# Optimization experiments

Measured on AMD Instinct MI355X. Metric: run time of the kernel, lower is better.

## Reference

```python
import jax, jax.numpy as jnp
import numpy as np

# static config (matches init_kwargs)
C = 64            # dim_split = dim // 4
DIM = 256
HID = 128         # int(dim//4 * mlp_ratio), mlp_ratio=2
S = 64            # state_dim
NH, HD = 16, 4    # GA: num_heads = C // head_dim, head_dim = 4
AK, AP = 11, 5    # att_kernel, att_padding
B, H, W = 8, 28, 28


def conv2d(x, w, pad, stride=1, groups=1, bias=None):
    out = jax.lax.conv_general_dilated(
        x, w, (stride, stride), pad, feature_group_count=groups,
        dimension_numbers=('NCHW', 'OIHW', 'NCHW'))
    if bias is not None:
        out = out + bias[None, :, None, None]
    return out


def pw(x, w, b=None):  # 1x1 conv, w: (O, Cin)
    y = jnp.einsum('oc,bchw->bohw', w, x)
    return y if b is None else y + b[None, :, None, None]


def bn(x, p, eps=1e-5):  # eval-mode BatchNorm2d; p: (4, C) = gamma, beta, mean, var
    g, b, m, v = p
    s = g / jnp.sqrt(v + eps)
    return (x - m[None, :, None, None]) * s[None, :, None, None] + b[None, :, None, None]


def relu6(x):
    return jnp.minimum(jax.nn.relu(x), 6.0)


def maxpool3(x):  # 3x3, stride 1, pad 1
    return jax.lax.reduce_window(x, -jnp.inf, jax.lax.max, (1, 1, 3, 3), (1, 1, 1, 1),
                                 [(0, 0), (0, 0), (1, 1), (1, 1)])


def blurpool(x):  # antialiased_cnns.BlurPool(channels, stride=3), filt_size=4
    a = np.array([1.0, 3.0, 3.0, 1.0])
    filt = np.outer(a, a)
    filt = filt / filt.sum()
    c = x.shape[1]
    w = jnp.asarray(np.tile(filt[None, None], (c, 1, 1, 1)), x.dtype)
    xp = jnp.pad(x, ((0, 0), (0, 0), (1, 2), (1, 2)), mode='reflect')
    return conv2d(xp, w, [(0, 0), (0, 0)], stride=3, groups=c)


def h_transform(x):
    b, c, hs, ws = x.shape
    x = jnp.pad(x, ((0, 0), (0, 0), (0, 0), (0, ws))).reshape(b, c, -1)[..., :-ws]
    return x.reshape(b, c, hs, 2 * ws - 1)


def inv_h_transform(x):
    b, c, hs, _ = x.shape
    x = jnp.pad(x.reshape(b, c, -1), ((0, 0), (0, 0), (0, hs)))
    return x.reshape(b, c, hs, 2 * hs)[..., :hs]


def v_transform(x):
    return h_transform(x.transpose(0, 1, 3, 2)).transpose(0, 1, 3, 2)


def inv_v_transform(x):
    return inv_h_transform(x.transpose(0, 1, 3, 2)).transpose(0, 1, 3, 2)


def _forward(x, dw1_w, dw1_b, bn_dw1, f1_w, f1_b, f2_w, f2_b, g_w, g_b, bn_g,
             dw2_w, dw2_b, hatt1_w, vatt1_w, hatt2_w, vatt2_w, bn_mra,
             bcdt_w, ssd_dw_w, hz_w, out_w, A_param, D_param,
             qkv_w, proj_w, bn_norm4, mlp1_w, bn_mlp, mlp2_w, bn_norm1):
    shortcut = x
    x1, x2, x3, x4 = jnp.split(x, 4, axis=1)

    # --- branch 1: dwconv + star-gated MLP ---
    x1o = bn(conv2d(x1, dw1_w, [(3, 3), (3, 3)], groups=C, bias=dw1_b), bn_dw1)
    x1 = relu6(pw(x1o, f1_w, f1_b)) * pw(x1o, f2_w, f2_b)
    x1 = conv2d(bn(pw(x1, g_w, g_b), bn_g), dw2_w, [(3, 3), (3, 3)], groups=C, bias=dw2_b)

    # --- branch 2: MRA ---
    xt = blurpool(maxpool3(x2))  # (B, C, 10, 10)
    xh1 = conv2d(xt, hatt1_w, [(AP, AP), (1, 1)], groups=C)
    xw1 = conv2d(xt, vatt1_w, [(1, 1), (AP, AP)], groups=C)
    xh2 = inv_h_transform(conv2d(h_transform(xt), hatt2_w, [(AP, AP), (1, 1)], groups=C))
    xw2 = inv_v_transform(conv2d(v_transform(xt), vatt2_w, [(1, 1), (AP, AP)], groups=C))
    att = jax.nn.sigmoid(bn(xh1 + xw1 + xh2 + xw2, bn_mra))
    hs, ws = att.shape[-2], att.shape[-1]
    ri = (jnp.arange(H) * hs) // H  # nearest-neighbor upsampling indices
    ci = (jnp.arange(W) * ws) // W
    x2 = x2 * att[:, :, ri][:, :, :, ci]

    # --- branch 3: HSMSSD (hidden-state-mixer SSD) ---
    L = H * W
    xs = x3.reshape(B, C, L)
    bcdt = conv2d(jnp.einsum('oc,bcl->bol', bcdt_w, xs).reshape(B, 3 * S, H, W),
                  ssd_dw_w, [(1, 1), (1, 1)], groups=3 * S).reshape(B, 3 * S, L)
    Bm, Cm, dt = jnp.split(bcdt, 3, axis=1)              # each (B, S, L)
    A = jax.nn.softmax(dt + A_param[None, :, None], axis=-1)
    h = jnp.einsum('bcl,bsl->bcs', xs, A * Bm)           # (B, C, S)
    h_, z = jnp.split(jnp.einsum('oc,bcs->bos', hz_w, h), 2, axis=1)
    h_ = jnp.einsum('oc,bcs->bos', out_w, h_ * jax.nn.silu(z) + h_ * D_param)
    x3 = jnp.einsum('bcs,bsl->bcl', h_, Cm).reshape(B, C, H, W)

    # --- branch 4: GA full attention + BN residual (stage == 3) ---
    t = x4.reshape(B, C, L).transpose(0, 2, 1)           # (B, N, C)
    qkv = (t @ qkv_w.T).reshape(B, L, 3, NH, HD).transpose(2, 0, 3, 1, 4)
    q, k, v = qkv[0], qkv[1], qkv[2]
    attn = jax.nn.softmax(jnp.einsum('bhnd,bhmd->bhnm', q, k) * HD ** -0.5, axis=-1)
    o = jnp.einsum('bhnm,bhmd->bhnd', attn, v).transpose(0, 2, 1, 3).reshape(B, L, NH * HD)
    x4 = bn(x4 + (o @ proj_w.T).transpose(0, 2, 1).reshape(B, C, H, W), bn_norm4)

    # --- merge + MLP ---
    xa = jnp.concatenate([x1, x2, x3, x4], axis=1)
    m = pw(jax.nn.relu(bn(pw(xa, mlp1_w), bn_mlp)), mlp2_w)
    return shortcut + bn(m, bn_norm1)


def setup_inputs() -> dict:
    key = jax.random.key(0)
    ks = iter(jax.random.split(key, 64))

    def w(shape, s=0.05):
        return jax.random.normal(next(ks), shape, dtype=jnp.float32) * s

    def bnp(c):
        g = 1.0 + 0.1 * jax.random.normal(next(ks), (c,), dtype=jnp.float32)
        b = 0.1 * jax.random.normal(next(ks), (c,), dtype=jnp.float32)
        m = 0.1 * jax.random.normal(next(ks), (c,), dtype=jnp.float32)
        v = 0.5 + jax.random.uniform(next(ks), (c,), dtype=jnp.float32)
        return jnp.stack([g, b, m, v])

    return dict(
        x=jax.random.normal(next(ks), (B, DIM, H, W), dtype=jnp.float32),
        dw1_w=w((C, 1, 7, 7), 0.1), dw1_b=w((C,), 0.02), bn_dw1=bnp(C),
        f1_w=w((HID, C)), f1_b=w((HID,), 0.02),
        f2_w=w((HID, C)), f2_b=w((HID,), 0.02),
        g_w=w((C, HID)), g_b=w((C,), 0.02), bn_g=bnp(C),
        dw2_w=w((C, 1, 7, 7), 0.1), dw2_b=w((C,), 0.02),
        hatt1_w=w((C, 1, AK, 3), 0.1), vatt1_w=w((C, 1, 3, AK), 0.1),
        hatt2_w=w((C, 1, AK, 3), 0.1), vatt2_w=w((C, 1, 3, AK), 0.1),
        bn_mra=bnp(C),
        bcdt_w=w((3 * S, C)), ssd_dw_w=w((3 * S, 1, 3, 3), 0.1),
        hz_w=w((2 * C, C)), out_w=w((C, C)),
        A_param=jax.random.uniform(next(ks), (S,), dtype=jnp.float32, minval=1.0, maxval=16.0),
        D_param=jnp.ones((1,), dtype=jnp.float32),
        qkv_w=w((3 * NH * HD, C)), proj_w=w((C, NH * HD)),
        bn_norm4=bnp(C),
        mlp1_w=w((HID, DIM)), bn_mlp=bnp(HID), mlp2_w=w((DIM, HID)),
        bn_norm1=bnp(DIM),
    )


def reference(x, dw1_w, dw1_b, bn_dw1, f1_w, f1_b, f2_w, f2_b, g_w, g_b, bn_g,
              dw2_w, dw2_b, hatt1_w, vatt1_w, hatt2_w, vatt2_w, bn_mra,
              bcdt_w, ssd_dw_w, hz_w, out_w, A_param, D_param,
              qkv_w, proj_w, bn_norm4, mlp1_w, bn_mlp, mlp2_w, bn_norm1):
    return _forward(x, dw1_w, dw1_b, bn_dw1, f1_w, f1_b, f2_w, f2_b, g_w, g_b, bn_g,
                    dw2_w, dw2_b, hatt1_w, vatt1_w, hatt2_w, vatt2_w, bn_mra,
                    bcdt_w, ssd_dw_w, hz_w, out_w, A_param, D_param,
                    qkv_w, proj_w, bn_norm4, mlp1_w, bn_mlp, mlp2_w, bn_norm1)
```

## Files before the change

kernel.cpp:

```cpp
#include <hip/hip_runtime.h>
#include <hip/hip_bf16.h>
#include <math.h>

#define DEV __device__ __forceinline__

constexpr int B=8, C=64, DIM=256, HID=128, S=64, NH=16, HD=4, LPIX=784;
constexpr int NPIX = B*LPIX;
constexpr int CH   = (NPIX+255)/256;
constexpr int QB   = 12*((NPIX+511)/512);

constexpr size_t OFF_X1O = 0;
constexpr size_t OFF_T1  = OFF_X1O + (size_t)B*C*LPIX;
constexpr size_t OFF_T2  = OFF_T1  + (size_t)B*HID*LPIX;
constexpr size_t OFF_XA  = OFF_T2  + (size_t)B*C*LPIX;
constexpr size_t OFF_BC2 = OFF_XA  + (size_t)B*DIM*LPIX;
constexpr size_t OFF_WGT = OFF_BC2 + (size_t)B*192*LPIX;
constexpr size_t OFF_H   = OFF_WGT + (size_t)B*S*LPIX;
constexpr size_t OFF_HO  = OFF_H   + (size_t)4*B*C*S;
constexpr size_t OFF_QKV = OFF_HO  + (size_t)B*C*S;
constexpr size_t OFF_O   = OFF_QKV + (size_t)3*B*NH*LPIX*HD;
constexpr size_t OFF_LS  = OFF_O   + (size_t)4*B*LPIX*C;
constexpr size_t OFF_MID = OFF_LS  + (size_t)4*B*NH*LPIX;

DEV float bnorm(float x, const float* p, int c, int nc){
  float g=p[c], bb=p[nc+c], m=p[2*nc+c], v=p[3*nc+c];
  return (x-m)*(g*rsqrtf(v+1e-5f))+bb;
}
DEV int refl(int p){ int k=p-1; if(k<0)k=-k; if(k>27)k=54-k; return k; }

DEV bool upix(int blk, int tid, int ngroups, int& grp, int& b, int& l){
  grp = blk % ngroups;
  int gidx = (blk/ngroups)*256 + tid;
  if(gidx >= NPIX) return false;
  b = gidx / LPIX; l = gidx % LPIX;
  return true;
}

DEV void body_dw1t(int bc, int tid, float* xs, const float* X, const float* w, const float* bias, const float* bnp, float* out){
  int c = bc & 63, b = bc >> 6;
  const float* xp = X + ((size_t)(b*DIM+c))*LPIX;
  for(int i=tid;i<34*34;i+=256) xs[i]=0.f;
  __syncthreads();
  for(int i=tid;i<LPIX;i+=256){ int y=i/28, x=i%28; xs[(y+3)*34+(x+3)]=xp[i]; }
  __syncthreads();
  const float* wc = w + (size_t)c*49;
  float bs = bias[c];
  for(int i=tid;i<LPIX;i+=256){
    int y=i/28, x=i%28;
    float s = bs;
    #pragma unroll
    for(int ky=0;ky<7;ky++){
      #pragma unroll
      for(int kx=0;kx<7;kx++)
        s += xs[(y+ky)*34 + x+kx]*wc[ky*7+kx];
    }
    out[((size_t)(b*C+c))*LPIX + i] = bnorm(s,bnp,c,C);
  }
}

DEV void body_branch2(int bc, int tid, float* smem, const float* X,
                      const float* h1w,const float* v1w,const float* h2w,const float* v2w,
                      const float* bnp, float* xa){
  int c = bc & 63, b = bc >> 6;
  float* xs  = smem;
  float* mp  = smem+LPIX;
  float* xt  = smem+2*LPIX;
  float* attv= smem+2*LPIX+100;
  const float* xp = X + ((size_t)(b*DIM+64+c))*LPIX;
  for(int i=tid;i<LPIX;i+=256) xs[i]=xp[i];
  __syncthreads();
  for(int i=tid;i<LPIX;i+=256){
    int y=i/28, x=i%28;
    float m=-1e30f;
    for(int dy=-1;dy<=1;dy++){ int iy=y+dy; if(iy<0||iy>=28) continue;
      for(int dx=-1;dx<=1;dx++){ int ix=x+dx; if(ix<0||ix>=28) continue;
        m=fmaxf(m,xs[iy*28+ix]); } }
    mp[i]=m;
  }
  __syncthreads();
  if(tid<100){
    int ii=tid/10, j=tid%10;
    const float fw[4]={0.125f,0.375f,0.375f,0.125f};
    float s=0;
    for(int ky=0;ky<4;ky++){ int rr=refl(3*ii+ky);
      for(int kx=0;kx<4;kx++){ int cc=refl(3*j+kx);
        s += fw[ky]*fw[kx]*mp[rr*28+cc]; } }
    xt[tid]=s;
  }
  __syncthreads();
  if(tid<100){
    int r=tid/10, j=tid%10;
    float s=0;
    for(int kh=0;kh<11;kh++){ int a=r+kh-5; if(a<0||a>=10) continue;
      for(int kw=0;kw<3;kw++){ int b2=j+kw-1; if(b2<0||b2>=10) continue;
        s+=xt[a*10+b2]*h1w[(size_t)c*33+kh*3+kw]; } }
    for(int kh=0;kh<3;kh++){ int a=r+kh-1; if(a<0||a>=10) continue;
      for(int kw=0;kw<11;kw++){ int b2=j+kw-5; if(b2<0||b2>=10) continue;
        s+=xt[a*10+b2]*v1w[(size_t)c*33+kh*11+kw]; } }
    { int t=20*r+j; int r2=t/19, j2=t%19;
      for(int kh=0;kh<11;kh++){ int a=r2+kh-5; if(a<0||a>=10) continue;
        for(int kw=0;kw<3;kw++){ int b2=j2+kw-1; if(b2<0||b2>=19) continue;
          int i2=19*a+b2; int row=i2/20, col=i2%20;
          if(col<10) s+=xt[row*10+col]*h2w[(size_t)c*33+kh*3+kw]; } } }
    { int t=20*j+r; int p=t%19, q=t/19;
      for(int kh=0;kh<3;kh++){ int a=p+kh-1; if(a<0||a>=19) continue;
        for(int kw=0;kw<11;kw++){ int b2=q+kw-5; if(b2<0||b2>=10) continue;
          int i2=19*b2+a; int row=i2/20, col=i2%20;
          if(col<10) s+=xt[col*10+row]*v2w[(size_t)c*33+kh*11+kw]; } } }
    s = bnorm(s,bnp,c,C);
    attv[tid] = 1.f/(1.f+__expf(-s));
  }
  __syncthreads();
  float* dst = xa + ((size_t)(b*DIM+64+c))*LPIX;
  for(int i=tid;i<LPIX;i+=256){
    int y=i/28, x=i%28;
    float a = attv[((y*10)/28)*10 + (x*10)/28];
    dst[i] = xs[i]*a;
  }
}

DEV void body_qkv(int blk, int tid, const float* X, const float* w, float* qkvb){
  int og = blk % 12;
  int p0 = (blk/12)*512 + tid;
  if(p0 >= NPIX) return;
  int o0 = og*16;
  int b0 = p0/LPIX, l0 = p0%LPIX;
  int p1 = p0 + 256;
  bool has1 = p1 < NPIX;
  int b1 = has1 ? p1/LPIX : b0, l1 = has1 ? p1%LPIX : l0;
  const float* xp0 = X + ((size_t)(b0*DIM+192))*LPIX + l0;
  const float* xp1 = X + ((size_t)(b1*DIM+192))*LPIX + l1;
  float s0[16], s1[16];
  #pragma unroll
  for(int t=0;t<16;t++){ s0[t]=0.f; s1[t]=0.f; }
  for(int c=0;c<C;c+=4){
    float a0=xp0[(size_t)c*LPIX],     a1=xp0[(size_t)(c+1)*LPIX],
          a2=xp0[(size_t)(c+2)*LPIX], a3=xp0[(size_t)(c+3)*LPIX];
    float e0=xp1[(size_t)c*LPIX],     e1=xp1[(size_t)(c+1)*LPIX],
          e2=xp1[(size_t)(c+2)*LPIX], e3=xp1[(size_t)(c+3)*LPIX];
    #pragma unroll
    for(int t=0;t<16;t++){
      const float* wr = w + (size_t)(o0+t)*C + c;
      float w0=wr[0], w1=wr[1], w2=wr[2], w3=wr[3];
      s0[t] += w0*a0 + w1*a1 + w2*a2 + w3*a3;
      s1[t] += w0*e0 + w1*e1 + w2*e2 + w3*e3;
    }
  }
  int which=o0>>6, head0=(o0&63)>>2;
  #pragma unroll
  for(int t4=0;t4<4;t4++){
    float4* dst = (float4*)(qkvb + (size_t)which*B*NH*LPIX*HD + ((size_t)((b0*NH+head0+t4)*LPIX+l0))*HD);
    *dst = make_float4(s0[4*t4],s0[4*t4+1],s0[4*t4+2],s0[4*t4+3]);
  }
  if(has1){
    #pragma unroll
    for(int t4=0;t4<4;t4++){
      float4* dst = (float4*)(qkvb + (size_t)which*B*NH*LPIX*HD + ((size_t)((b1*NH+head0+t4)*LPIX+l1))*HD);
      *dst = make_float4(s1[4*t4],s1[4*t4+1],s1[4*t4+2],s1[4*t4+3]);
    }
  }
}

DEV void body_bcdtssd(int blk, int tid, float* smem, const float* X, const float* w, const float* dww,
                      float* bc2, float* wgt){
  int b = blk/48, og = blk%48; int o0=og*4;
  float* bc1s = smem;
  float* dts1 = smem + 4*LPIX;
  float* red  = smem + 5*LPIX;
  const float* xp = X + ((size_t)(b*DIM+128))*LPIX;
  {
    int l0=tid, l1=tid+256, l2=tid+512;
    float acc0[4]={0,0,0,0}, acc1[4]={0,0,0,0}, acc2[4]={0,0,0,0};
    for(int c=0;c<C;c+=4){
      float x00=xp[(size_t)c*LPIX+l0],     x01=xp[(size_t)(c+1)*LPIX+l0],
            x02=xp[(size_t)(c+2)*LPIX+l0], x03=xp[(size_t)(c+3)*LPIX+l0];
      float x10=xp[(size_t)c*LPIX+l1],     x11=xp[(size_t)(c+1)*LPIX+l1],
            x12=xp[(size_t)(c+2)*LPIX+l1], x13=xp[(size_t)(c+3)*LPIX+l1];
      float x20=xp[(size_t)c*LPIX+l2],     x21=xp[(size_t)(c+1)*LPIX+l2],
            x22=xp[(size_t)(c+2)*LPIX+l2], x23=xp[(size_t)(c+3)*LPIX+l2];
      #pragma unroll
      for(int t=0;t<4;t++){
        const float* wr = w + (size_t)(o0+t)*C + c;
        float w0=wr[0], w1=wr[1], w2=wr[2], w3=wr[3];
        acc0[t] += w0*x00 + w1*x01 + w2*x02 + w3*x03;
        acc1[t] += w0*x10 + w1*x11 + w2*x12 + w3*x13;
        acc2[t] += w0*x20 + w1*x21 + w2*x22 + w3*x23;
      }
    }
    #pragma unroll
    for(int t=0;t<4;t++){
      bc1s[t*LPIX+l0]=acc0[t];
      bc1s[t*LPIX+l1]=acc1[t];
      bc1s[t*LPIX+l2]=acc2[t];
    }
    if(tid<16){
      int l=768+tid;
      float a0=0,a1=0,a2=0,a3=0;
      for(int c=0;c<C;c+=4){
        float x0=xp[(size_t)c*LPIX+l],     x1=xp[(size_t)(c+1)*LPIX+l],
              x2=xp[(size_t)(c+2)*LPIX+l], x3=xp[(size_t)(c+3)*LPIX+l];
        const float* w0p = w + (size_t)(o0+0)*C + c;
        const float* w1p = w + (size_t)(o0+1)*C + c;
        const float* w2p = w + (size_t)(o0+2)*C + c;
        const float* w3p = w + (size_t)(o0+3)*C + c;
        a0 += w0p[0]*x0 + w0p[1]*x1 + w0p[2]*x2 + w0p[3]*x3;
        a1 += w1p[0]*x0 + w1p[1]*x1 + w1p[2]*x2 + w1p[3]*x3;
        a2 += w2p[0]*x0 + w2p[1]*x1 + w2p[2]*x2 + w2p[3]*x3;
        a3 += w3p[0]*x0 + w3p[1]*x1 + w3p[2]*x2 + w3p[3]*x3;
      }
      bc1s[0*LPIX+l]=a0; bc1s[1*LPIX+l]=a1; bc1s[2*LPIX+l]=a2; bc1s[3*LPIX+l]=a3;
    }
  }
  __syncthreads();
  if(og < 32){
    for(int i=tid;i<4*LPIX;i+=256){
      int oo=i/LPIX, l=i%LPIX; int y=l/28, x=l%28;
      const float* p = bc1s + oo*LPIX;
      const float* wk = dww + (size_t)(o0+oo)*9;
      float s=0;
      for(int ky=0;ky<3;ky++){ int iy=y+ky-1; if(iy<0||iy>=28) continue;
        for(int kx=0;kx<3;kx++){ int ix=x+kx-1; if(ix<0||ix>=28) continue;
          s += p[iy*28+ix]*wk[ky*3+kx]; } }
      bc2[((size_t)(b*192+o0+oo))*LPIX + l] = s;
    }
  } else {
    int wv = tid>>6, lane = tid&63;
    for(int oo=0;oo<4;oo++){
      const float* p = bc1s + oo*LPIX;
      const float* wk = dww + (size_t)(o0+oo)*9;
      float lmax=-1e30f;
      for(int i=tid;i<LPIX;i+=256){
        int y=i/28, x=i%28;
        float s=0;
        for(int ky=0;ky<3;ky++){ int iy=y+ky-1; if(iy<0||iy>=28) continue;
          for(int kx=0;kx<3;kx++){ int ix=x+kx-1; if(ix<0||ix>=28) continue;
            s += p[iy*28+ix]*wk[ky*3+kx]; } }
        dts1[i]=s;
        lmax=fmaxf(lmax,s);
      }
      for(int off=32;off;off>>=1) lmax=fmaxf(lmax,__shfl_xor(lmax,off));
      if(lane==0) red[wv]=lmax;
      __syncthreads();
      float bmax = fmaxf(fmaxf(red[0],red[1]),fmaxf(red[2],red[3]));
      float lsum=0;
      for(int i=tid;i<LPIX;i+=256){
        float e=__expf(dts1[i]-bmax);
        dts1[i]=e; lsum+=e;
      }
      for(int off=32;off;off>>=1) lsum += __shfl_xor(lsum,off);
      if(lane==0) red[4+wv]=lsum;
      __syncthreads();
      float inv = 1.f/(red[4]+red[5]+red[6]+red[7]);
      int s_ = o0-128+oo;
      float* wp = wgt + ((size_t)(b*S+s_))*LPIX;
      for(int i=tid;i<LPIX;i+=256) wp[i] = dts1[i]*inv;
      __syncthreads();
    }
  }
}

DEV void body_attn(int blk, int tid, float4* ks, float4* vs, const float* qkvb,
                   float* ob, float* lsb){
  int bh = blk >> 2, ms = blk & 3;
  int b = bh>>4, h = bh&15;
  const float4* q4 = (const float4*)(qkvb + (size_t)bh*LPIX*HD);
  const float4* k4 = (const float4*)(qkvb + (size_t)(B*NH + bh)*LPIX*HD) + ms*196;
  const float4* v4 = (const float4*)(qkvb + (size_t)(2*B*NH + bh)*LPIX*HD) + ms*196;
  for(int i=tid;i<196;i+=256){ ks[i]=k4[i]; vs[i]=v4[i]; }
  __syncthreads();
  const float SC = 0.5f*1.44269504f;
  float* obp = ob + (size_t)ms*B*LPIX*C;
  float* lsq = lsb + (size_t)ms*B*NH*LPIX + (size_t)bh*LPIX;

  float4 q[3];
  #pragma unroll
  for(int j=0;j<3;j++){
    float4 t = q4[tid + 256*j];
    q[j] = make_float4(t.x*SC, t.y*SC, t.z*SC, t.w*SC);
  }
  float l0[3]={0,0,0}, l1[3]={0,0,0};
  float ax0[3]={0,0,0}, ax1[3]={0,0,0};
  float ay0[3]={0,0,0}, ay1[3]={0,0,0};
  float az0[3]={0,0,0}, az1[3]={0,0,0};
  float aw0[3]={0,0,0}, aw1[3]={0,0,0};
  for(int m=0;m<196;m+=2){
    float4 k0=ks[m], k1=ks[m+1];
    float4 v0=vs[m], v1=vs[m+1];
    #pragma unroll
    for(int j=0;j<3;j++){
      float s0 = q[j].x*k0.x + q[j].y*k0.y + q[j].z*k0.z + q[j].w*k0.w;
      float s1 = q[j].x*k1.x + q[j].y*k1.y + q[j].z*k1.z + q[j].w*k1.w;
      float p0 = __builtin_amdgcn_exp2f(s0);
      float p1 = __builtin_amdgcn_exp2f(s1);
      l0[j]+=p0;        l1[j]+=p1;
      ax0[j]+=p0*v0.x;  ax1[j]+=p1*v1.x;
      ay0[j]+=p0*v0.y;  ay1[j]+=p1*v1.y;
      az0[j]+=p0*v0.z;  az1[j]+=p1*v1.z;
      aw0[j]+=p0*v0.w;  aw1[j]+=p1*v1.w;
    }
  }
  #pragma unroll
  for(int j=0;j<3;j++){
    int r = tid + 256*j;
    *(float4*)(obp + ((size_t)(b*LPIX+r))*C + h*4) =
        make_float4(ax0[j]+ax1[j], ay0[j]+ay1[j], az0[j]+az1[j], aw0[j]+aw1[j]);
    lsq[r] = l0[j]+l1[j];
  }
  if(tid < 16){
    int r = 768 + tid;
    float4 t = q4[r];
    float4 qq = make_float4(t.x*SC,t.y*SC,t.z*SC,t.w*SC);
    float ls=0; float4 a=make_float4(0,0,0,0);
    for(int m=0;m<196;m++){
      float4 kv=ks[m], vv=vs[m];
      float sc = qq.x*kv.x+qq.y*kv.y+qq.z*kv.z+qq.w*kv.w;
      float p = __builtin_amdgcn_exp2f(sc);
      ls+=p; a.x+=p*vv.x; a.y+=p*vv.y; a.z+=p*vv.z; a.w+=p*vv.w;
    }
    *(float4*)(obp + ((size_t)(b*LPIX+r))*C + h*4) = a;
    lsq[r] = ls;
  }
}

DEV void body_star(int blk, int tid, const float* x1o, const float* f1w,const float* f1b,const float* f2w,const float* f2b,float* t1){
  int jg, b, l; if(!upix(blk, tid, 32, jg, b, l)) return;
  int j0=jg*4;
  const float* xp = x1o + (size_t)b*C*LPIX + l;
  float a[4], g[4];
  for(int t=0;t<4;t++){ a[t]=f1b[j0+t]; g[t]=f2b[j0+t]; }
  for(int c=0;c<C;c++){
    float xv = xp[(size_t)c*LPIX];
    for(int t=0;t<4;t++){ a[t]+=f1w[(size_t)(j0+t)*C+c]*xv; g[t]+=f2w[(size_t)(j0+t)*C+c]*xv; }
  }
  for(int t=0;t<4;t++){
    float av = fminf(fmaxf(a[t],0.f),6.f);
    t1[((size_t)(b*HID+j0+t))*LPIX + l] = av*g[t];
  }
}

DEV void body_gproj(int blk, int tid, const float* t1, const float* gw,const float* gb,const float* bnp,float* t2){
  int cg, b, l; if(!upix(blk, tid, 4, cg, b, l)) return;
  int c0=cg*16;
  const float* tp = t1 + (size_t)b*HID*LPIX + l;
  float s[16];
  #pragma unroll
  for(int t=0;t<16;t++) s[t]=gb[c0+t];
  for(int j=0;j<HID;j++){
    float xv = tp[(size_t)j*LPIX];
    #pragma unroll
    for(int t=0;t<16;t++) s[t]+=gw[(size_t)(c0+t)*HID+j]*xv;
  }
  #pragma unroll
  for(int t=0;t<16;t++) t2[((size_t)(b*C+c0+t))*LPIX + l]=bnorm(s[t],bnp,c0+t,C);
}

DEV void body_x4(int blk, int tid, const float* X, const float* ob, const float* lsb,
                 const float* projw, const float* bnp, float* xa){
  int cg, b, l; if(!upix(blk, tid, 4, cg, b, l)) return;
  int c0=cg*16;
  const float* p0 = ob + ((size_t)(b*LPIX+l))*C;
  const float* p1 = p0 + (size_t)B*LPIX*C;
  const float* p2 = p1 + (size_t)B*LPIX*C;
  const float* p3 = p2 + (size_t)B*LPIX*C;
  float s[16];
  #pragma unroll
  for(int t=0;t<16;t++) s[t]=0.f;
  for(int h=0;h<NH;h++){
    size_t li = ((size_t)(b*NH+h))*LPIX + l;
    float lsum = lsb[li] + lsb[(size_t)B*NH*LPIX+li] + lsb[(size_t)2*B*NH*LPIX+li] + lsb[(size_t)3*B*NH*LPIX+li];
    float iv = 1.f/lsum;
    float4 q0=*(const float4*)(p0+h*4), q1=*(const float4*)(p1+h*4),
           q2=*(const float4*)(p2+h*4), q3=*(const float4*)(p3+h*4);
    float ov0=(q0.x+q1.x+q2.x+q3.x)*iv;
    float ov1=(q0.y+q1.y+q2.y+q3.y)*iv;
    float ov2=(q0.z+q1.z+q2.z+q3.z)*iv;
    float ov3=(q0.w+q1.w+q2.w+q3.w)*iv;
    const float* pw = projw + h*4;
    #pragma unroll
    for(int t=0;t<16;t++){
      const float* pr = pw + (size_t)(c0+t)*C;
      s[t] += pr[0]*ov0 + pr[1]*ov1 + pr[2]*ov2 + pr[3]*ov3;
    }
  }
  #pragma unroll
  for(int t=0;t<16;t++){
    float v = s[t] + X[((size_t)(b*DIM+192+c0+t))*LPIX + l];
    xa[((size_t)(b*DIM+192+c0+t))*LPIX + l] = bnorm(v,bnp,c0+t,C);
  }
}

DEV void body_h(int blk, int tid, float* smem, const float* X, const float* wgt, const float* bc2, float* hq){
  int b = blk >> 6, sub = blk & 63;
  int tile = sub >> 2, qq = sub & 3;
  int ct = (tile>>2)*16, st = (tile&3)*16;
  float (*Xs)[99] = (float(*)[99])smem;
  float (*Ws)[99] = (float(*)[99])(smem + 16*99);
  int tc = tid>>4, ts = tid&15;
  float acc=0;
  #pragma unroll
  for(int half=0;half<2;half++){
    int lb = qq*196 + half*98;
    for(int i=tid;i<16*98;i+=256){
      int r=i/98, col=i%98;
      Xs[r][col] = X[((size_t)(b*DIM+128+ct+r))*LPIX + lb + col];
      Ws[r][col] = wgt[((size_t)(b*S+st+r))*LPIX + lb + col]
                 * bc2[((size_t)(b*192+st+r))*LPIX + lb + col];
    }
    __syncthreads();
    #pragma unroll 7
    for(int l=0;l<98;l++) acc += Xs[tc][l]*Ws[ts][l];
    __syncthreads();
  }
  hq[(size_t)qq*B*C*S + ((size_t)(b*C+ct+tc))*S + st+ts] = acc;
}

DEV void body_dw2t(int bc, int tid, float* xs, const float* t2, const float* w, const float* bias, float* xa){
  int c = bc & 63, b = bc >> 6;
  const float* tp = t2 + ((size_t)(b*C+c))*LPIX;
  for(int i=tid;i<34*34;i+=256) xs[i]=0.f;
  __syncthreads();
  for(int i=tid;i<LPIX;i+=256){ int y=i/28, x=i%28; xs[(y+3)*34+(x+3)]=tp[i]; }
  __syncthreads();
  const float* wc = w + (size_t)c*49;
  float bs = bias[c];
  for(int i=tid;i<LPIX;i+=256){
    int y=i/28, x=i%28;
    float s = bs;
    #pragma unroll
    for(int ky=0;ky<7;ky++){
      #pragma unroll
      for(int kx=0;kx<7;kx++)
        s += xs[(y+ky)*34 + x+kx]*wc[ky*7+kx];
    }
    xa[((size_t)(b*DIM+c))*LPIX + i] = s;
  }
}

DEV void body_mixho(int blk, int tid, float* smem, const float* hq, const float* hzw,
                    const float* Dp, const float* outw, float* ho){
  int b = blk >> 3, st = (blk & 7) * 8;
  float (*hs2)[8] = (float(*)[8])smem;
  float (*g1s)[8] = (float(*)[8])(smem + C*8);
  for(int i=tid;i<C*8;i+=256){
    int k=i>>3, si=i&7;
    size_t off = ((size_t)(b*C+k))*S + st + si;
    hs2[k][si] = hq[off] + hq[(size_t)B*C*S+off] + hq[(size_t)2*B*C*S+off] + hq[(size_t)3*B*C*S+off];
  }
  __syncthreads();
  float D = Dp[0];
  for(int i=tid;i<C*8;i+=256){
    int c=i>>3, si=i&7;
    float hv=0, zv=0;
    for(int k=0;k<C;k++){ float x=hs2[k][si]; hv+=hzw[(size_t)c*C+k]*x; zv+=hzw[(size_t)(C+c)*C+k]*x; }
    float sil = zv/(1.f+__expf(-zv));
    g1s[c][si]=hv*sil+hv*D;
  }
  __syncthreads();
  for(int i=tid;i<C*8;i+=256){
    int c=i>>3, si=i&7;
    float acc=0;
    for(int k=0;k<C;k++) acc+=outw[(size_t)c*C+k]*g1s[k][si];
    ho[((size_t)(b*C+c))*S + st + si]=acc;
  }
}

DEV void body_x3(int blk, int tid, const float* ho, const float* bc2, float* xa){
  int cg, b, l; if(!upix(blk, tid, 16, cg, b, l)) return;
  int c0=cg*4;
  const float* hp = ho + (size_t)(b*C+c0)*S;
  const float* cm = bc2 + ((size_t)(b*192+64))*LPIX + l;
  float s[4]={0,0,0,0};
  for(int s_=0;s_<S;s_++){
    float cv = cm[(size_t)s_*LPIX];
    for(int t=0;t<4;t++) s[t] += hp[(size_t)t*S+s_]*cv;
  }
  for(int t=0;t<4;t++)
    xa[((size_t)(b*DIM+128+c0+t))*LPIX + l] = s[t];
}

__global__ void k_s1(const float* X,
                     const float* bcdt_w, const float* ssd_dw, float* bc2, float* wgt,
                     const float* h1w,const float* v1w,const float* h2w,const float* v2w,const float* bn_mra,
                     const float* qkv_w, float* qkvb,
                     const float* dw1_w,const float* dw1_b,const float* bn_dw1,
                     float* xa, float* x1o){
  __shared__ float smem[5*LPIX+8];
  int blk = blockIdx.x, tid = threadIdx.x;
  if(blk < 384)            body_bcdtssd(blk, tid, smem, X, bcdt_w, ssd_dw, bc2, wgt);
  else if(blk < 896)       body_branch2(blk-384, tid, smem, X, h1w,v1w,h2w,v2w, bn_mra, xa);
  else if(blk < 896+QB)    body_qkv(blk-896, tid, X, qkv_w, qkvb);
  else                     body_dw1t(blk-(896+QB), tid, smem, X, dw1_w, dw1_b, bn_dw1, x1o);
}

__global__ void k_s2(const float* qkvb, float* ob, float* lsb,
                     const float* x1o, const float* f1w,const float* f1b,const float* f2w,const float* f2b, float* t1,
                     const float* X, const float* wgt, const float* bc2, float* hq){
  __shared__ float4 smem4[792];
  float* smem = (float*)smem4;
  int blk = blockIdx.x, tid = threadIdx.x;
  if(blk < 512)            body_attn(blk, tid, smem4, smem4+196, qkvb, ob, lsb);
  else if(blk < 512+32*CH) body_star(blk-512, tid, x1o, f1w,f1b,f2w,f2b, t1);
  else                     body_h(blk-(512+32*CH), tid, smem, X, wgt, bc2, hq);
}

__global__ void k_s3(const float* t1, const float* gw,const float* gb,const float* bn_g, float* t2,
                     const float* X, const float* ob, const float* lsb,
                     const float* projw, const float* bn_n4, float* xa,
                     const float* hq, const float* hzw, const float* Dp, const float* outw, float* ho){
  __shared__ float smem[2*C*8];
  int blk = blockIdx.x, tid = threadIdx.x;
  if(blk < 64)           body_mixho(blk, tid, smem, hq, hzw, Dp, outw, ho);
  else if(blk < 64+4*CH) body_gproj(blk-64, tid, t1, gw, gb, bn_g, t2);
  else                   body_x4(blk-(64+4*CH), tid, X, ob, lsb, projw, bn_n4, xa);
}

__global__ void k_s4(const float* t2, const float* dw2_w, const float* dw2_b, float* xa,
                     const float* ho, const float* bc2){
  __shared__ float smem[34*34];
  int blk = blockIdx.x, tid = threadIdx.x;
  if(blk < 512) body_dw2t(blk, tid, smem, t2, dw2_w, dw2_b, xa);
  else          body_x3(blk-512, tid, ho, bc2, xa);
}

__global__ void k_mid(const float* xa, const float* m1w, const float* bnp, float* mid){
  int jg, b, l; if(!upix(blockIdx.x, threadIdx.x, 32, jg, b, l)) return;
  int j0=jg*4;
  const float* xp = xa + (size_t)b*DIM*LPIX + l;
  float s[4]={0,0,0,0};
  for(int c=0;c<DIM;c++){
    float xv=xp[(size_t)c*LPIX];
    for(int t=0;t<4;t++) s[t]+=m1w[(size_t)(j0+t)*DIM+c]*xv;
  }
  for(int t=0;t<4;t++)
    mid[((size_t)(b*HID+j0+t))*LPIX + l] = fmaxf(bnorm(s[t],bnp,j0+t,HID),0.f);
}

__global__ void k_out(const float* X, const float* mid, const float* m2w, const float* bnp, float* out){
  int cg, b, l; if(!upix(blockIdx.x, threadIdx.x, 32, cg, b, l)) return;
  int c0=cg*8;
  const float* mp_ = mid + (size_t)b*HID*LPIX + l;
  float s[8]={0,0,0,0,0,0,0,0};
  for(int j=0;j<HID;j++){
    float mv=mp_[(size_t)j*LPIX];
    for(int t=0;t<8;t++) s[t]+=m2w[(size_t)(c0+t)*HID+j]*mv;
  }
  for(int t=0;t<8;t++){
    size_t oi = ((size_t)(b*DIM+c0+t))*LPIX + l;
    out[oi] = bnorm(s[t],bnp,c0+t,DIM) + X[oi];
  }
}

extern "C" void kernel_launch(void* const* d_in, const int* in_sizes, int n_in,
                              void* d_out, int out_size, void* d_ws, size_t ws_size,
                              hipStream_t stream) {
  const float* X      = (const float*)d_in[0];
  const float* dw1_w  = (const float*)d_in[1];
  const float* dw1_b  = (const float*)d_in[2];
  const float* bn_dw1 = (const float*)d_in[3];
  const float* f1_w   = (const float*)d_in[4];
  const float* f1_b   = (const float*)d_in[5];
  const float* f2_w   = (const float*)d_in[6];
  const float* f2_b   = (const float*)d_in[7];
  const float* g_w    = (const float*)d_in[8];
  const float* g_b    = (const float*)d_in[9];
  const float* bn_g   = (const float*)d_in[10];
  const float* dw2_w  = (const float*)d_in[11];
  const float* dw2_b  = (const float*)d_in[12];
  const float* hatt1w = (const float*)d_in[13];
  const float* vatt1w = (const float*)d_in[14];
  const float* hatt2w = (const float*)d_in[15];
  const float* vatt2w = (const float*)d_in[16];
  const float* bn_mra = (const float*)d_in[17];
  const float* bcdt_w = (const float*)d_in[18];
  const float* ssd_dw = (const float*)d_in[19];
  const float* hz_w   = (const float*)d_in[20];
  const float* out_w  = (const float*)d_in[21];
  const float* D_p    = (const float*)d_in[23];
  const float* qkv_w  = (const float*)d_in[24];
  const float* proj_w = (const float*)d_in[25];
  const float* bn_n4  = (const float*)d_in[26];
  const float* mlp1_w = (const float*)d_in[27];
  const float* bn_mlp = (const float*)d_in[28];
  const float* mlp2_w = (const float*)d_in[29];
  const float* bn_n1  = (const float*)d_in[30];

  float* ws   = (float*)d_ws;
  float* x1o  = ws+OFF_X1O;  float* t1  = ws+OFF_T1;  float* t2  = ws+OFF_T2;
  float* xa   = ws+OFF_XA;   float* bc2 = ws+OFF_BC2; float* wgt = ws+OFF_WGT;
  float* hq   = ws+OFF_H;    float* ho  = ws+OFF_HO;  float* qkvb= ws+OFF_QKV;
  float* ob   = ws+OFF_O;    float* lsb = ws+OFF_LS;  float* mid = ws+OFF_MID;

  dim3 blk(256);

  k_s1 <<<dim3(896+QB+512),blk,0,stream>>>(X, bcdt_w, ssd_dw, bc2, wgt,
                                     hatt1w,vatt1w,hatt2w,vatt2w,bn_mra,
                                     qkv_w, qkvb, dw1_w,dw1_b,bn_dw1, xa, x1o);
  k_s2 <<<dim3(512+32*CH+512),blk,0,stream>>>(qkvb, ob, lsb,
                                     x1o, f1_w,f1_b,f2_w,f2_b, t1,
                                     X, wgt, bc2, hq);
  k_s3 <<<dim3(64+8*CH),blk,0,stream>>>(t1, g_w,g_b,bn_g, t2,
                                     X, ob, lsb, proj_w, bn_n4, xa,
                                     hq, hz_w, D_p, out_w, ho);
  k_s4 <<<dim3(512+16*CH),blk,0,stream>>>(t2, dw2_w, dw2_b, xa, ho, bc2);
  k_mid<<<dim3(32*CH),blk,0,stream>>>(xa,mlp1_w,bn_mlp,mid);
  k_out<<<dim3(32*CH),blk,0,stream>>>(X,mid,mlp2_w,bn_n1,(float*)d_out);
}
```

Measured before the change: 283.8 us.

## Parallelize softmax per wavefront, unroll channel loops, widen x3 per-thread outputs

The softmax branch of the bcdt/ssd stage used to run its four channels one after another, with block-wide reductions and several barriers per channel. It now computes all four depthwise convolutions up front, keeps them in shared memory, and gives each wavefront one channel to reduce with shuffles only. Shared memory for that kernel drops from 5 to 4 planes. Separately, the star, mid and out pointwise loops are manually unrolled by 4 in the input channel, and body_x3 computes 8 output channels per thread instead of 4, halving its block count. These aim to cut barrier overhead and per-element load overhead, in exchange for more registers per thread.

New measurement: 276.6 us. 1.03x faster.

```diff
diff --git a/kernel.cpp b/kernel.cpp
--- a/kernel.cpp
+++ b/kernel.cpp
@@ -165,8 +165,6 @@
                       float* bc2, float* wgt){
   int b = blk/48, og = blk%48; int o0=og*4;
   float* bc1s = smem;
-  float* dts1 = smem + 4*LPIX;
-  float* red  = smem + 5*LPIX;
   const float* xp = X + ((size_t)(b*DIM+128))*LPIX;
   {
     int l0=tid, l1=tid+256, l2=tid+512;
@@ -224,38 +222,37 @@
       bc2[((size_t)(b*192+o0+oo))*LPIX + l] = s;
     }
   } else {
-    int wv = tid>>6, lane = tid&63;
-    for(int oo=0;oo<4;oo++){
-      const float* p = bc1s + oo*LPIX;
-      const float* wk = dww + (size_t)(o0+oo)*9;
-      float lmax=-1e30f;
-      for(int i=tid;i<LPIX;i+=256){
-        int y=i/28, x=i%28;
+    float cv[13];
+    #pragma unroll
+    for(int k=0;k<13;k++){
+      int i = tid + k*256;
+      if(i < 4*LPIX){
+        int oo=i/LPIX, l=i%LPIX; int y=l/28, x=l%28;
+        const float* p = bc1s + oo*LPIX;
+        const float* wk = dww + (size_t)(o0+oo)*9;
         float s=0;
         for(int ky=0;ky<3;ky++){ int iy=y+ky-1; if(iy<0||iy>=28) continue;
           for(int kx=0;kx<3;kx++){ int ix=x+kx-1; if(ix<0||ix>=28) continue;
             s += p[iy*28+ix]*wk[ky*3+kx]; } }
-        dts1[i]=s;
-        lmax=fmaxf(lmax,s);
+        cv[k]=s;
       }
-      for(int off=32;off;off>>=1) lmax=fmaxf(lmax,__shfl_xor(lmax,off));
-      if(lane==0) red[wv]=lmax;
-      __syncthreads();
-      float bmax = fmaxf(fmaxf(red[0],red[1]),fmaxf(red[2],red[3]));
-      float lsum=0;
-      for(int i=tid;i<LPIX;i+=256){
-        float e=__expf(dts1[i]-bmax);
-        dts1[i]=e; lsum+=e;
-      }
-      for(int off=32;off;off>>=1) lsum += __shfl_xor(lsum,off);
-      if(lane==0) red[4+wv]=lsum;
-      __syncthreads();
-      float inv = 1.f/(red[4]+red[5]+red[6]+red[7]);
-      int s_ = o0-128+oo;
-      float* wp = wgt + ((size_t)(b*S+s_))*LPIX;
-      for(int i=tid;i<LPIX;i+=256) wp[i] = dts1[i]*inv;
-      __syncthreads();
-    }
+    }
+    __syncthreads();
+    #pragma unroll
+    for(int k=0;k<13;k++){ int i=tid+k*256; if(i<4*LPIX) bc1s[i]=cv[k]; }
+    __syncthreads();
+    int wv = tid>>6, lane = tid&63;
+    float* row = bc1s + wv*LPIX;
+    float mx = -1e30f;
+    for(int l=lane;l<LPIX;l+=64) mx = fmaxf(mx, row[l]);
+    for(int off=32;off;off>>=1) mx = fmaxf(mx, __shfl_xor(mx,off));
+    float sum=0;
+    for(int l=lane;l<LPIX;l+=64){ float e=__expf(row[l]-mx); row[l]=e; sum+=e; }
+    for(int off=32;off;off>>=1) sum += __shfl_xor(sum,off);
+    float inv = 1.f/sum;
+    int s_ = o0-128+wv;
+    float* wp = wgt + ((size_t)(b*S+s_))*LPIX;
+    for(int l=lane;l<LPIX;l+=64) wp[l] = row[l]*inv;
   }
 }
 
@@ -328,9 +325,16 @@
   const float* xp = x1o + (size_t)b*C*LPIX + l;
   float a[4], g[4];
   for(int t=0;t<4;t++){ a[t]=f1b[j0+t]; g[t]=f2b[j0+t]; }
-  for(int c=0;c<C;c++){
-    float xv = xp[(size_t)c*LPIX];
-    for(int t=0;t<4;t++){ a[t]+=f1w[(size_t)(j0+t)*C+c]*xv; g[t]+=f2w[(size_t)(j0+t)*C+c]*xv; }
+  for(int c=0;c<C;c+=4){
+    float x0=xp[(size_t)c*LPIX],     x1=xp[(size_t)(c+1)*LPIX],
+          x2=xp[(size_t)(c+2)*LPIX], x3=xp[(size_t)(c+3)*LPIX];
+    #pragma unroll
+    for(int t=0;t<4;t++){
+      const float* f1r = f1w + (size_t)(j0+t)*C + c;
+      const float* f2r = f2w + (size_t)(j0+t)*C + c;
+      a[t] += f1r[0]*x0 + f1r[1]*x1 + f1r[2]*x2 + f1r[3]*x3;
+      g[t] += f2r[0]*x0 + f2r[1]*x1 + f2r[2]*x2 + f2r[3]*x3;
+    }
   }
   for(int t=0;t<4;t++){
     float av = fminf(fmaxf(a[t],0.f),6.f);
@@ -465,16 +469,22 @@
 }
 
 DEV void body_x3(int blk, int tid, const float* ho, const float* bc2, float* xa){
-  int cg, b, l; if(!upix(blk, tid, 16, cg, b, l)) return;
-  int c0=cg*4;
+  int cg, b, l; if(!upix(blk, tid, 8, cg, b, l)) return;
+  int c0=cg*8;
   const float* hp = ho + (size_t)(b*C+c0)*S;
   const float* cm = bc2 + ((size_t)(b*192+64))*LPIX + l;
-  float s[4]={0,0,0,0};
-  for(int s_=0;s_<S;s_++){
-    float cv = cm[(size_t)s_*LPIX];
-    for(int t=0;t<4;t++) s[t] += hp[(size_t)t*S+s_]*cv;
-  }
-  for(int t=0;t<4;t++)
+  float s[8];
+  #pragma unroll
+  for(int t=0;t<8;t++) s[t]=0.f;
+  for(int s_=0;s_<S;s_+=2){
+    float cv0 = cm[(size_t)s_*LPIX];
+    float cv1 = cm[(size_t)(s_+1)*LPIX];
+    #pragma unroll
+    for(int t=0;t<8;t++)
+      s[t] += hp[(size_t)t*S+s_]*cv0 + hp[(size_t)t*S+s_+1]*cv1;
+  }
+  #pragma unroll
+  for(int t=0;t<8;t++)
     xa[((size_t)(b*DIM+128+c0+t))*LPIX + l] = s[t];
 }
 
@@ -484,7 +494,7 @@
                      const float* qkv_w, float* qkvb,
                      const float* dw1_w,const float* dw1_b,const float* bn_dw1,
                      float* xa, float* x1o){
-  __shared__ float smem[5*LPIX+8];
+  __shared__ float smem[4*LPIX];
   int blk = blockIdx.x, tid = threadIdx.x;
   if(blk < 384)            body_bcdtssd(blk, tid, smem, X, bcdt_w, ssd_dw, bc2, wgt);
   else if(blk < 896)       body_branch2(blk-384, tid, smem, X, h1w,v1w,h2w,v2w, bn_mra, xa);
@@ -527,9 +537,14 @@
   int j0=jg*4;
   const float* xp = xa + (size_t)b*DIM*LPIX + l;
   float s[4]={0,0,0,0};
-  for(int c=0;c<DIM;c++){
-    float xv=xp[(size_t)c*LPIX];
-    for(int t=0;t<4;t++) s[t]+=m1w[(size_t)(j0+t)*DIM+c]*xv;
+  for(int c=0;c<DIM;c+=4){
+    float x0=xp[(size_t)c*LPIX],     x1=xp[(size_t)(c+1)*LPIX],
+          x2=xp[(size_t)(c+2)*LPIX], x3=xp[(size_t)(c+3)*LPIX];
+    #pragma unroll
+    for(int t=0;t<4;t++){
+      const float* wr = m1w + (size_t)(j0+t)*DIM + c;
+      s[t] += wr[0]*x0 + wr[1]*x1 + wr[2]*x2 + wr[3]*x3;
+    }
   }
   for(int t=0;t<4;t++)
     mid[((size_t)(b*HID+j0+t))*LPIX + l] = fmaxf(bnorm(s[t],bnp,j0+t,HID),0.f);
@@ -540,9 +555,14 @@
   int c0=cg*8;
   const float* mp_ = mid + (size_t)b*HID*LPIX + l;
   float s[8]={0,0,0,0,0,0,0,0};
-  for(int j=0;j<HID;j++){
-    float mv=mp_[(size_t)j*LPIX];
-    for(int t=0;t<8;t++) s[t]+=m2w[(size_t)(c0+t)*HID+j]*mv;
+  for(int j=0;j<HID;j+=4){
+    float m0=mp_[(size_t)j*LPIX],     m1=mp_[(size_t)(j+1)*LPIX],
+          m2=mp_[(size_t)(j+2)*LPIX], m3=mp_[(size_t)(j+3)*LPIX];
+    #pragma unroll
+    for(int t=0;t<8;t++){
+      const float* wr = m2w + (size_t)(c0+t)*HID + j;
+      s[t] += wr[0]*m0 + wr[1]*m1 + wr[2]*m2 + wr[3]*m3;
+    }
   }
   for(int t=0;t<8;t++){
     size_t oi = ((size_t)(b*DIM+c0+t))*LPIX + l;
@@ -601,7 +621,7 @@
   k_s3 <<<dim3(64+8*CH),blk,0,stream>>>(t1, g_w,g_b,bn_g, t2,
                                      X, ob, lsb, proj_w, bn_n4, xa,
                                      hq, hz_w, D_p, out_w, ho);
-  k_s4 <<<dim3(512+16*CH),blk,0,stream>>>(t2, dw2_w, dw2_b, xa, ho, bc2);
+  k_s4 <<<dim3(512+8*CH),blk,0,stream>>>(t2, dw2_w, dw2_b, xa, ho, bc2);
   k_mid<<<dim3(32*CH),blk,0,stream>>>(xa,mlp1_w,bn_mlp,mid);
   k_out<<<dim3(32*CH),blk,0,stream>>>(X,mid,mlp2_w,bn_n1,(float*)d_out);
 }
```
